# Optimization experiments

Hardware: AMD Instinct MI355X
Metric: run time of the kernel (lower is better)

Reference implementation:

```python
import jax, jax.numpy as jnp
import numpy as np

IN_F = 1024   # in_features
OUT_F = 1024  # out_features
N = 32768     # flattened batch (prod of x.shape[:-1]))
K = 3         # clones per rewire -> denom = K + 1


def setup_inputs() -> dict:
    key = jax.random.key(0)
    k1, k2, k3, k4 = jax.random.split(key, 4)
    bound = 1.0 / np.sqrt(IN_F)
    x = jax.random.normal(k1, (N, IN_F), dtype=jnp.float32)
    # kaiming-uniform-ish init scale for weight, uniform(-bound,bound) for bias
    weight = jax.random.uniform(k2, (OUT_F, IN_F), dtype=jnp.float32,
                                minval=-bound, maxval=bound) * np.sqrt(3.0)
    bias = jax.random.uniform(k3, (OUT_F,), dtype=jnp.float32,
                              minval=-bound, maxval=bound)
    # one rewire per output row; clones are distinct from src (dead-neuron slots)
    rewire_rows = jnp.arange(OUT_F, dtype=jnp.int32)
    rewire_src = jax.random.randint(k4, (OUT_F,), 0, IN_F, dtype=jnp.int32)
    rewire_clones = (rewire_src[:, None] + jnp.arange(1, K + 1, dtype=jnp.int32)) % IN_F
    return {"x": x, "weight": weight, "bias": bias,
            "rewire_rows": rewire_rows, "rewire_src": rewire_src,
            "rewire_clones": rewire_clones}


def reference(x, weight, bias, rewire_rows, rewire_src, rewire_clones):
    # Plain linear part, shared by all output rows: y = x @ W^T + b
    base = x @ weight.T + bias                                  # [N, OUT_F]

    # Per-rewire correction. For rewire e on row r with src s and clones d_k
    # (denom = K+1), the torch loop replaces x[:, s] -> x[:, s]/denom and
    # x[:, d_k] -> x[:, s]/denom before the GEMV with weight[r].
    # Equivalent delta added to base[:, r] (indices within a rewire are disjoint):
    denom = rewire_clones.shape[1] + 1                          # K + 1
    xs = x[:, rewire_src]                                       # [N, R]
    new_val = xs / denom                                        # [N, R]
    w_src = weight[rewire_rows, rewire_src]                     # [R]
    delta = (new_val - xs) * w_src                              # src column change
    xc = x[:, rewire_clones]                                    # [N, R, K]
    wc = weight[rewire_rows[:, None], rewire_clones]            # [R, K]
    delta = delta + jnp.einsum('nrk,rk->nr', new_val[:, :, None] - xc, wc)

    # Scatter-add the deltas into their output rows (duplicates accumulate).
    return base.at[:, rewire_rows].add(delta)                   # [N, OUT_F]
```

## Files before the change

### kernel.cpp

```cpp
#include <hip/hip_runtime.h>

#define IN_F 1024
#define OUT_F 1024
#define NTOK 32768
#define BM 256
#define BN 256
#define BK 64
#define KT (IN_F / BK)

typedef __bf16 bf16;
typedef __bf16 bf16x4 __attribute__((ext_vector_type(4)));
typedef __bf16 bf16x8 __attribute__((ext_vector_type(8)));
typedef float f32x4 __attribute__((ext_vector_type(4)));

__global__ void build_wp(const float* __restrict__ W,
                         const int* __restrict__ rows,
                         const int* __restrict__ srcs,
                         const int* __restrict__ clones,
                         bf16* __restrict__ Wp) {
  const int r = blockIdx.x;
  const int row = rows[r];
  const int s = srcs[r];
  const int c0 = clones[3 * r + 0];
  const int c1 = clones[3 * r + 1];
  const int c2 = clones[3 * r + 2];
  const float* wr = W + (size_t)row * IN_F;
  const float fixv = 0.25f * (wr[s] + wr[c0] + wr[c1] + wr[c2]);

  const int col = threadIdx.x * 4;
  f32x4 v = *reinterpret_cast<const f32x4*>(wr + col);
  bf16x4 o;
#pragma unroll
  for (int j = 0; j < 4; ++j) {
    const int c = col + j;
    float f = v[j];
    if (c == c0 || c == c1 || c == c2) f = 0.0f;
    if (c == s) f = fixv;
    o[j] = (bf16)f;
  }
  *reinterpret_cast<bf16x4*>(Wp + (size_t)row * IN_F + col) = o;
}

__global__ void prep_xb(const float* __restrict__ X, bf16* __restrict__ Xb) {
  const int c = blockIdx.x * 256 + threadIdx.x;
  const int q = c & 2047;
  const int bmt = c >> 11;
  const int bm = bmt >> 4;
  const int t = bmt & 15;
  const int row = q >> 3;
  const int p = q & 7;
  const int s = p ^ (row & 7);
  const float* src = X + ((size_t)bm * BM + row) * IN_F + t * BK + s * 8;
  const f32x4 a = *reinterpret_cast<const f32x4*>(src);
  const f32x4 b = *reinterpret_cast<const f32x4*>(src + 4);
  bf16x8 o;
#pragma unroll
  for (int j = 0; j < 4; ++j) {
    o[j] = (bf16)a[j];
    o[4 + j] = (bf16)b[j];
  }
  *reinterpret_cast<bf16x8*>(Xb + (size_t)c * 8) = o;
}

__global__ __launch_bounds__(512, 1) void gemm_bf(
    const bf16* __restrict__ Xb, const bf16* __restrict__ Wp,
    const float* __restrict__ bias, float* __restrict__ out) {
  extern __shared__ __align__(16) char smem[];

  const int tid = threadIdx.x;
  const int lane = tid & 63;
  const int w = tid >> 6;
  const int wrow = w >> 2;
  const int wcol = w & 3;

  const int bid = blockIdx.x;
  const int sq = bid >> 3;
  const int bm = (bid & 7) + 8 * (sq >> 2);
  const int bn = sq & 3;

  const bf16* gA = Xb + (size_t)bm * (KT * 16384) + lane * 8;

  const bf16* gB = Wp + ((size_t)bn * BN + w * 8 + (lane >> 3)) * IN_F +
                   (((lane & 7) ^ ((lane >> 3) & 7)) * 8);

  f32x4 acc[8][4];
#pragma unroll
  for (int n = 0; n < 4; ++n) {
    const float bv = bias[bn * BN + wcol * 64 + n * 16 + (lane & 15)];
#pragma unroll
    for (int m = 0; m < 8; ++m) acc[m][n] = (f32x4){bv, bv, bv, bv};
  }

  const int rl = lane & 15;
  const int rx = rl & 7;
  const int arow0 = wrow * 128 + rl;
  const int brow0 = wcol * 64 + rl;
  const int sl0 = lane >> 4;

  auto issueA = [&](int t, int slot) {
    const bf16* g = gA + (size_t)t * 16384;
#pragma unroll
    for (int i = 0; i < 4; ++i) {
      const int chunk = i * 8 + w;
      __builtin_amdgcn_global_load_lds(
          (const __attribute__((address_space(1))) void*)(g + chunk * 512),
          (__attribute__((address_space(3))) void*)(smem + slot * 32768 +
                                                    chunk * 1024),
          16, 0, 0);
    }
  };
  auto issueB = [&](int t, int slot) {
    const bf16* g = gB + (size_t)t * BK;
    char* dst0 = smem + 98304 + slot * 32768 + w * 1024;
#pragma unroll
    for (int i = 0; i < 4; ++i) {
      __builtin_amdgcn_global_load_lds(
          (const __attribute__((address_space(1))) void*)(g +
                                                          (size_t)i * 64 * IN_F),
          (__attribute__((address_space(3))) void*)(dst0 + i * 8192), 16, 0, 0);
    }
  };
  auto compute = [&](int t) {
    const char* A = smem + (t % 3) * 32768;
    const char* B = smem + 98304 + (t & 1) * 32768;
#pragma unroll
    for (int kk = 0; kk < 2; ++kk) {
      const int so = (((kk * 4 + sl0) ^ rx) << 4);
      bf16x8 af[8], bfr[4];
#pragma unroll
      for (int m = 0; m < 8; ++m)
        af[m] =
            *reinterpret_cast<const bf16x8*>(A + (arow0 + m * 16) * 128 + so);
#pragma unroll
      for (int n = 0; n < 4; ++n)
        bfr[n] =
            *reinterpret_cast<const bf16x8*>(B + (brow0 + n * 16) * 128 + so);
      __builtin_amdgcn_s_setprio(1);
#pragma unroll
      for (int m = 0; m < 8; ++m)
#pragma unroll
        for (int n = 0; n < 4; ++n)
          acc[m][n] = __builtin_amdgcn_mfma_f32_16x16x32_bf16(
              af[m], bfr[n], acc[m][n], 0, 0, 0);
      __builtin_amdgcn_s_setprio(0);
    }
  };

  issueB(0, 0);
  issueA(0, 0);
  issueA(1, 1);
  asm volatile("s_waitcnt vmcnt(4)" ::: "memory");
  __builtin_amdgcn_s_barrier();
  __builtin_amdgcn_sched_barrier(0);

  for (int t = 0; t < KT; ++t) {
    if (t + 1 < KT) issueB(t + 1, (t + 1) & 1);
    if (t + 2 < KT) issueA(t + 2, (t + 2) % 3);
    __builtin_amdgcn_sched_barrier(0);
    compute(t);
    if (t + 1 < KT) {
      if (t + 2 < KT)
        asm volatile("s_waitcnt vmcnt(4)" ::: "memory");
      else
        asm volatile("s_waitcnt vmcnt(0)" ::: "memory");
      __builtin_amdgcn_s_barrier();
      __builtin_amdgcn_sched_barrier(0);
    }
  }

  const int orow0 = bm * BM + wrow * 128 + (lane >> 4) * 4;
  const int ocol = bn * BN + wcol * 64 + (lane & 15);
#pragma unroll
  for (int m = 0; m < 8; ++m) {
#pragma unroll
    for (int n = 0; n < 4; ++n) {
      const f32x4 v = acc[m][n];
      const size_t base = (size_t)(orow0 + m * 16) * OUT_F + (ocol + n * 16);
#pragma unroll
      for (int i = 0; i < 4; ++i) out[base + (size_t)i * OUT_F] = v[i];
    }
  }
}

__global__ __launch_bounds__(512, 2) void gemm_r4(
    const float* __restrict__ X, const bf16* __restrict__ Wp,
    const float* __restrict__ bias, float* __restrict__ out) {
  extern __shared__ __align__(16) char smem[];

  const int tid = threadIdx.x;
  const int lane = tid & 63;
  const int w = tid >> 6;
  const int wrow = w >> 2;
  const int wcol = w & 3;

  const int bid = blockIdx.x;
  const int sq = bid >> 3;
  const int bm = (bid & 7) + 8 * (sq >> 2);
  const int bn = sq & 3;

  const float* gA = X + ((size_t)bm * BM + (tid >> 3)) * IN_F + (tid & 7) * 8;
  const int awbyte =
      ((tid >> 3) << 7) + ((((tid & 7) ^ ((tid >> 3) & 7))) << 4);

  const bf16* gB = Wp + ((size_t)bn * BN + w * 8 + (lane >> 3)) * IN_F +
                   (((lane & 7) ^ ((lane >> 3) & 7)) * 8);

  f32x4 acc[8][4];
#pragma unroll
  for (int n = 0; n < 4; ++n) {
    const float bv = bias[bn * BN + wcol * 64 + n * 16 + (lane & 15)];
#pragma unroll
    for (int m = 0; m < 8; ++m) acc[m][n] = (f32x4){bv, bv, bv, bv};
  }

  const int rl = lane & 15;
  const int rx = rl & 7;
  const int arow0 = wrow * 128 + rl;
  const int brow0 = wcol * 64 + rl;
  const int sl0 = lane >> 4;

  f32x4 av[8];

  auto issueA = [&](int t) {
#pragma unroll
    for (int j = 0; j < 4; ++j) {
      const float* p = gA + (size_t)j * 64 * IN_F + (size_t)t * BK;
      av[2 * j] = *reinterpret_cast<const f32x4*>(p);
      av[2 * j + 1] = *reinterpret_cast<const f32x4*>(p + 4);
    }
  };
  auto writeA = [&](int buf) {
    char* base = smem + buf * 32768;
#pragma unroll
    for (int j = 0; j < 4; ++j) {
      bf16x8 o;
#pragma unroll
      for (int q = 0; q < 4; ++q) {
        o[q] = (bf16)av[2 * j][q];
        o[4 + q] = (bf16)av[2 * j + 1][q];
      }
      *reinterpret_cast<bf16x8*>(base + j * 8192 + awbyte) = o;
    }
  };
  auto issueB = [&](int t, int buf) {
    const bf16* g = gB + (size_t)t * BK;
    char* dst0 = smem + 65536 + buf * 32768 + w * 1024;
#pragma unroll
    for (int i = 0; i < 4; ++i) {
      __builtin_amdgcn_global_load_lds(
          (const __attribute__((address_space(1))) void*)(g +
                                                          (size_t)i * 64 * IN_F),
          (__attribute__((address_space(3))) void*)(dst0 + i * 8192), 16, 0, 0);
    }
  };
  auto compute = [&](int buf) {
    const char* A = smem + buf * 32768;
    const char* B = smem + 65536 + buf * 32768;
#pragma unroll
    for (int kk = 0; kk < 2; ++kk) {
      const int so = (((kk * 4 + sl0) ^ rx) << 4);
      bf16x8 af[8], bfr[4];
#pragma unroll
      for (int m = 0; m < 8; ++m)
        af[m] =
            *reinterpret_cast<const bf16x8*>(A + (arow0 + m * 16) * 128 + so);
#pragma unroll
      for (int n = 0; n < 4; ++n)
        bfr[n] =
            *reinterpret_cast<const bf16x8*>(B + (brow0 + n * 16) * 128 + so);
      __builtin_amdgcn_s_setprio(1);
#pragma unroll
      for (int m = 0; m < 8; ++m)
#pragma unroll
        for (int n = 0; n < 4; ++n)
          acc[m][n] = __builtin_amdgcn_mfma_f32_16x16x32_bf16(
              af[m], bfr[n], acc[m][n], 0, 0, 0);
      __builtin_amdgcn_s_setprio(0);
    }
  };

  issueA(0);
  issueB(0, 0);
  writeA(0);
  __syncthreads();

  for (int t = 0; t < KT; ++t) {
    const int db = t & 1;
    const bool more = (t + 1) < KT;
    if (more) {
      issueA(t + 1);
      issueB(t + 1, db ^ 1);
      __builtin_amdgcn_sched_barrier(0);
    }
    compute(db);
    if (more) {
      __builtin_amdgcn_sched_barrier(0);
      writeA(db ^ 1);
      __syncthreads();
    }
  }

  const int orow0 = bm * BM + wrow * 128 + (lane >> 4) * 4;
  const int ocol = bn * BN + wcol * 64 + (lane & 15);
#pragma unroll
  for (int m = 0; m < 8; ++m) {
#pragma unroll
    for (int n = 0; n < 4; ++n) {
      const f32x4 v = acc[m][n];
      const size_t base = (size_t)(orow0 + m * 16) * OUT_F + (ocol + n * 16);
#pragma unroll
      for (int i = 0; i < 4; ++i) out[base + (size_t)i * OUT_F] = v[i];
    }
  }
}

extern "C" void kernel_launch(void* const* d_in, const int* in_sizes, int n_in,
                              void* d_out, int out_size, void* d_ws,
                              size_t ws_size, hipStream_t stream) {
  const float* x = (const float*)d_in[0];
  const float* weight = (const float*)d_in[1];
  const float* bias = (const float*)d_in[2];
  const int* rrows = (const int*)d_in[3];
  const int* rsrc = (const int*)d_in[4];
  const int* rclones = (const int*)d_in[5];
  float* out = (float*)d_out;

  bf16* Wp = (bf16*)d_ws;
  bf16* Xb = (bf16*)((char*)d_ws + (2u << 20));
  const size_t need = (2u << 20) + (size_t)NTOK * IN_F * 2;

  (void)hipFuncSetAttribute((const void*)gemm_bf,
                            hipFuncAttributeMaxDynamicSharedMemorySize, 163840);
  (void)hipFuncSetAttribute((const void*)gemm_r4,
                            hipFuncAttributeMaxDynamicSharedMemorySize, 131072);

  build_wp<<<dim3(OUT_F), dim3(256), 0, stream>>>(weight, rrows, rsrc, rclones,
                                                  Wp);
  if (ws_size >= need) {
    prep_xb<<<dim3((NTOK / BM) * KT * 2048 / 256), dim3(256), 0, stream>>>(x,
                                                                           Xb);
    gemm_bf<<<dim3((NTOK / BM) * (OUT_F / BN)), dim3(512), 163840, stream>>>(
        Xb, Wp, bias, out);
  } else {
    gemm_r4<<<dim3((NTOK / BM) * (OUT_F / BN)), dim3(512), 131072, stream>>>(
        x, Wp, bias, out);
  }
}
```

Baseline: 116.9 us.

## Halve GEMM k-tile to 32 with triple-buffered A/B and split-phase interleaved loads

Halves the bf16 GEMM k-step from 64 to 32 and triple-buffers both the A and B tiles in 96KB of LDS, down from 160KB. The pre-swizzled X layout in prep_xb changes to match the 64-byte rows. Each k-step is split into two halves of 16 MFMAs, with the global-to-LDS prefetch of A issued in the first half and B in the second, separated by barriers. The aim is to overlap loads with math more finely and cut LDS use, at the cost of twice as many k iterations and extra barriers per step.

```diff
diff --git a/kernel.cpp b/kernel.cpp
--- a/kernel.cpp
+++ b/kernel.cpp
@@ -6,7 +6,9 @@
 #define BM 256
 #define BN 256
 #define BK 64
-#define KT (IN_F / BK)
+#define KT 16
+#define BK2 32
+#define KT2 32
 
 typedef __bf16 bf16;
 typedef __bf16 bf16x4 __attribute__((ext_vector_type(4)));
@@ -43,14 +45,14 @@
 
 __global__ void prep_xb(const float* __restrict__ X, bf16* __restrict__ Xb) {
   const int c = blockIdx.x * 256 + threadIdx.x;
-  const int q = c & 2047;
-  const int bmt = c >> 11;
-  const int bm = bmt >> 4;
-  const int t = bmt & 15;
-  const int row = q >> 3;
-  const int p = q & 7;
-  const int s = p ^ (row & 7);
-  const float* src = X + ((size_t)bm * BM + row) * IN_F + t * BK + s * 8;
+  const int q = c & 1023;
+  const int img = c >> 10;
+  const int bm = img >> 5;
+  const int t = img & 31;
+  const int row = q >> 2;
+  const int p = q & 3;
+  const int s = p ^ ((row >> 1) & 3);
+  const float* src = X + ((size_t)bm * BM + row) * IN_F + t * BK2 + s * 8;
   const f32x4 a = *reinterpret_cast<const f32x4*>(src);
   const f32x4 b = *reinterpret_cast<const f32x4*>(src + 4);
   bf16x8 o;
@@ -78,10 +80,10 @@
   const int bm = (bid & 7) + 8 * (sq >> 2);
   const int bn = sq & 3;
 
-  const bf16* gA = Xb + (size_t)bm * (KT * 16384) + lane * 8;
-
-  const bf16* gB = Wp + ((size_t)bn * BN + w * 8 + (lane >> 3)) * IN_F +
-                   (((lane & 7) ^ ((lane >> 3) & 7)) * 8);
+  const bf16* gA = Xb + (size_t)bm * (KT2 * 8192) + lane * 8;
+
+  const bf16* gB = Wp + ((size_t)bn * BN + (lane >> 2)) * IN_F +
+                   (((lane & 3) ^ ((lane >> 3) & 3)) * 8);
 
   f32x4 acc[8][4];
 #pragma unroll
@@ -92,80 +94,103 @@
   }
 
   const int rl = lane & 15;
-  const int rx = rl & 7;
+  const int xr = (rl >> 1) & 3;
   const int arow0 = wrow * 128 + rl;
   const int brow0 = wcol * 64 + rl;
-  const int sl0 = lane >> 4;
-
-  auto issueA = [&](int t, int slot) {
-    const bf16* g = gA + (size_t)t * 16384;
-#pragma unroll
-    for (int i = 0; i < 4; ++i) {
-      const int chunk = i * 8 + w;
-      __builtin_amdgcn_global_load_lds(
-          (const __attribute__((address_space(1))) void*)(g + chunk * 512),
-          (__attribute__((address_space(3))) void*)(smem + slot * 32768 +
-                                                    chunk * 1024),
-          16, 0, 0);
-    }
-  };
-  auto issueB = [&](int t, int slot) {
-    const bf16* g = gB + (size_t)t * BK;
-    char* dst0 = smem + 98304 + slot * 32768 + w * 1024;
-#pragma unroll
-    for (int i = 0; i < 4; ++i) {
-      __builtin_amdgcn_global_load_lds(
-          (const __attribute__((address_space(1))) void*)(g +
-                                                          (size_t)i * 64 * IN_F),
-          (__attribute__((address_space(3))) void*)(dst0 + i * 8192), 16, 0, 0);
-    }
-  };
-  auto compute = [&](int t) {
-    const char* A = smem + (t % 3) * 32768;
-    const char* B = smem + 98304 + (t & 1) * 32768;
-#pragma unroll
-    for (int kk = 0; kk < 2; ++kk) {
-      const int so = (((kk * 4 + sl0) ^ rx) << 4);
-      bf16x8 af[8], bfr[4];
-#pragma unroll
-      for (int m = 0; m < 8; ++m)
-        af[m] =
-            *reinterpret_cast<const bf16x8*>(A + (arow0 + m * 16) * 128 + so);
+  const int so = ((lane >> 4) ^ xr) << 4;
+
+  auto gloadA = [&](int t, int i) {
+    const int chunk = w + i * 8;
+    __builtin_amdgcn_global_load_lds(
+        (const __attribute__((address_space(1))) void*)(gA + (size_t)t * 8192 +
+                                                        chunk * 512),
+        (__attribute__((address_space(3))) void*)(smem + (t % 3) * 16384 +
+                                                  chunk * 1024),
+        16, 0, 0);
+  };
+  auto gloadB = [&](int t, int i) {
+    const int chunk = w + i * 8;
+    __builtin_amdgcn_global_load_lds(
+        (const __attribute__((address_space(1))) void*)(gB +
+                                                        (size_t)chunk * 16 *
+                                                            IN_F +
+                                                        t * BK2),
+        (__attribute__((address_space(3))) void*)(smem + 49152 +
+                                                  (t % 3) * 16384 +
+                                                  chunk * 1024),
+        16, 0, 0);
+  };
+
+  bf16x8 bfr[4];
+  auto readB = [&](int t) {
+    const char* B = smem + 49152 + (t % 3) * 16384;
+#pragma unroll
+    for (int n = 0; n < 4; ++n)
+      bfr[n] = *reinterpret_cast<const bf16x8*>(B + (brow0 + n * 16) * 64 + so);
+  };
+  auto readA4 = [&](int t, int m0, bf16x8 (&af)[4]) {
+    const char* A = smem + (t % 3) * 16384;
+#pragma unroll
+    for (int dm = 0; dm < 4; ++dm)
+      af[dm] = *reinterpret_cast<const bf16x8*>(A + (arow0 + (m0 + dm) * 16) *
+                                                        64 +
+                                                    so);
+  };
+  auto mfma16 = [&](const bf16x8 (&af)[4], int m0) {
+    __builtin_amdgcn_s_setprio(1);
+#pragma unroll
+    for (int dm = 0; dm < 4; ++dm)
 #pragma unroll
       for (int n = 0; n < 4; ++n)
-        bfr[n] =
-            *reinterpret_cast<const bf16x8*>(B + (brow0 + n * 16) * 128 + so);
-      __builtin_amdgcn_s_setprio(1);
-#pragma unroll
-      for (int m = 0; m < 8; ++m)
-#pragma unroll
-        for (int n = 0; n < 4; ++n)
-          acc[m][n] = __builtin_amdgcn_mfma_f32_16x16x32_bf16(
-              af[m], bfr[n], acc[m][n], 0, 0, 0);
-      __builtin_amdgcn_s_setprio(0);
-    }
-  };
-
-  issueB(0, 0);
-  issueA(0, 0);
-  issueA(1, 1);
+        acc[m0 + dm][n] = __builtin_amdgcn_mfma_f32_16x16x32_bf16(
+            af[dm], bfr[n], acc[m0 + dm][n], 0, 0, 0);
+    __builtin_amdgcn_s_setprio(0);
+  };
+
+#pragma unroll
+  for (int i = 0; i < 2; ++i) {
+    gloadA(0, i);
+    gloadB(0, i);
+  }
+#pragma unroll
+  for (int i = 0; i < 2; ++i) {
+    gloadA(1, i);
+    gloadB(1, i);
+  }
   asm volatile("s_waitcnt vmcnt(4)" ::: "memory");
   __builtin_amdgcn_s_barrier();
-  __builtin_amdgcn_sched_barrier(0);
-
-  for (int t = 0; t < KT; ++t) {
-    if (t + 1 < KT) issueB(t + 1, (t + 1) & 1);
-    if (t + 2 < KT) issueA(t + 2, (t + 2) % 3);
+
+#pragma unroll 1
+  for (int t = 0; t < KT2; ++t) {
+    const bool pf = (t + 2) < KT2;
+    bf16x8 af[4];
+    readB(t);
+    readA4(t, 0, af);
+    if (pf) {
+      gloadA(t + 2, 0);
+      gloadA(t + 2, 1);
+    }
+    __builtin_amdgcn_s_barrier();
+    asm volatile("s_waitcnt lgkmcnt(0)" ::: "memory");
     __builtin_amdgcn_sched_barrier(0);
-    compute(t);
-    if (t + 1 < KT) {
-      if (t + 2 < KT)
+    mfma16(af, 0);
+    __builtin_amdgcn_s_barrier();
+    readA4(t, 4, af);
+    if (pf) {
+      gloadB(t + 2, 0);
+      gloadB(t + 2, 1);
+    }
+    __builtin_amdgcn_s_barrier();
+    asm volatile("s_waitcnt lgkmcnt(0)" ::: "memory");
+    __builtin_amdgcn_sched_barrier(0);
+    mfma16(af, 4);
+    if (t + 1 < KT2) {
+      if (pf)
         asm volatile("s_waitcnt vmcnt(4)" ::: "memory");
       else
         asm volatile("s_waitcnt vmcnt(0)" ::: "memory");
-      __builtin_amdgcn_s_barrier();
-      __builtin_amdgcn_sched_barrier(0);
-    }
+    }
+    __builtin_amdgcn_s_barrier();
   }
 
   const int orow0 = bm * BM + wrow * 128 + (lane >> 4) * 4;
@@ -330,16 +355,15 @@
   const size_t need = (2u << 20) + (size_t)NTOK * IN_F * 2;
 
   (void)hipFuncSetAttribute((const void*)gemm_bf,
-                            hipFuncAttributeMaxDynamicSharedMemorySize, 163840);
+                            hipFuncAttributeMaxDynamicSharedMemorySize, 98304);
   (void)hipFuncSetAttribute((const void*)gemm_r4,
                             hipFuncAttributeMaxDynamicSharedMemorySize, 131072);
 
   build_wp<<<dim3(OUT_F), dim3(256), 0, stream>>>(weight, rrows, rsrc, rclones,
                                                   Wp);
   if (ws_size >= need) {
-    prep_xb<<<dim3((NTOK / BM) * KT * 2048 / 256), dim3(256), 0, stream>>>(x,
-                                                                           Xb);
-    gemm_bf<<<dim3((NTOK / BM) * (OUT_F / BN)), dim3(512), 163840, stream>>>(
+    prep_xb<<<dim3(16384), dim3(256), 0, stream>>>(x, Xb);
+    gemm_bf<<<dim3((NTOK / BM) * (OUT_F / BN)), dim3(512), 98304, stream>>>(
         Xb, Wp, bias, out);
   } else {
     gemm_r4<<<dim3((NTOK / BM) * (OUT_F / BN)), dim3(512), 131072, stream>>>(
```

Result: slower. 127.7 us (+9.3%).
